# Optimization experiments

Measured on AMD Instinct MI355X. Metric: run time of the kernel, lower is better.

The kernel has to match this reference:

```python
import jax, jax.numpy as jnp
import numpy as np
from jax import lax

D = 768
H = 12
L = 12
FF = 4 * D
SCALE = D ** -0.5  # NOTE: original scales by embed_dim**-0.5, not head_dim**-0.5
LN_EPS = 1e-5


def _layernorm(x, g, b):
    mu = jnp.mean(x, axis=-1, keepdims=True)
    var = jnp.mean(jnp.square(x - mu), axis=-1, keepdims=True)
    return (x - mu) * lax.rsqrt(var + LN_EPS) * g + b


def setup_inputs() -> dict:
    key = jax.random.key(0)
    ks = jax.random.split(key, 8)
    x = jax.random.normal(ks[0], (4, 1024, D), dtype=jnp.float32)
    s = 0.02
    Wq = s * jax.random.normal(ks[1], (L, D, D), dtype=jnp.float32)
    Wv = s * jax.random.normal(ks[2], (L, D, D), dtype=jnp.float32)
    Wo = s * jax.random.normal(ks[3], (L, D, D), dtype=jnp.float32)
    W1 = s * jax.random.normal(ks[4], (L, D, FF), dtype=jnp.float32)
    W2 = s * jax.random.normal(ks[5], (L, FF, D), dtype=jnp.float32)
    zD = jnp.zeros((L, D), dtype=jnp.float32)
    return {
        'x': x,
        'ln1_g': jnp.ones((L, D), jnp.float32), 'ln1_b': zD,
        'Wq': Wq, 'bq': zD, 'Wv': Wv, 'bv': zD, 'Wo': Wo, 'bo': zD,
        'ln2_g': jnp.ones((L, D), jnp.float32), 'ln2_b': zD,
        'W1': W1, 'b1': jnp.zeros((L, FF), jnp.float32),
        'W2': W2, 'b2': zD,
    }


def _block(x, p):
    ln1_g, ln1_b, Wq, bq, Wv, bv, Wo, bo, ln2_g, ln2_b, W1, b1, W2, b2 = p
    B, T, _ = x.shape
    h = _layernorm(x, ln1_g, ln1_b)
    # Faithful to source: scores use query vs VALUE (fc_k output is dead code)
    q = (h @ Wq + bq).reshape(B, T, H, D // H)
    v = (h @ Wv + bv).reshape(B, T, H, D // H)
    scores = jnp.einsum('blhd,bthd->bhlt', q, v) * SCALE
    probs = jax.nn.softmax(scores, axis=-1)
    ctx = jnp.einsum('bhlt,bthd->blhd', probs, v).reshape(B, T, D)
    skip = x + ctx @ Wo + bo
    h2 = _layernorm(skip, ln2_g, ln2_b)
    ff = jax.nn.gelu(h2 @ W1 + b1, approximate=False) @ W2 + b2
    return skip + ff


def reference(x, ln1_g, ln1_b, Wq, bq, Wv, bv, Wo, bo, ln2_g, ln2_b, W1, b1, W2, b2):
    params = (ln1_g, ln1_b, Wq, bq, Wv, bv, Wo, bo, ln2_g, ln2_b, W1, b1, W2, b2)
    out, _ = lax.scan(lambda c, p: (_block(c, p), None), x, params)
    return out
```

## Files before the change

### kernel.cpp

```cpp
#include <hip/hip_runtime.h>
#include <math.h>

#define BB 4
#define TT 1024
#define DD 768
#define HH 12
#define DH 64
#define FF2 3072
#define NL 12
#define MM (BB * TT)
#define SCALE 0.03608439182435161f
#define LN_EPS 1e-5f

typedef __attribute__((ext_vector_type(8))) short bf16x8;
typedef __attribute__((ext_vector_type(4))) float f32x4;

__device__ __forceinline__ ushort f2b(float x) {
    uint u = __float_as_uint(x);
    uint r = (u + 0x7fffu + ((u >> 16) & 1u)) >> 16;
    return (ushort)r;
}
__device__ __forceinline__ float b2f(ushort h) { return __uint_as_float(((uint)h) << 16); }

__device__ __forceinline__ float gelu_exact(float x) {
    return 0.5f * x * (1.0f + erff(x * 0.70710678118654752440f));
}

__device__ __forceinline__ int swz(int r, int q) {
    return 4 * r + ((q ^ (r & 3) ^ ((r >> 2) & 3)) & 3);
}

__device__ __forceinline__ void gl_lds16(const ushort* g, ushort* l) {
    __builtin_amdgcn_global_load_lds(
        (__attribute__((address_space(1))) void*)(g),
        (__attribute__((address_space(3))) void*)(l), 16, 0, 0);
}

__global__ __launch_bounds__(256) void ln_kernel(const float* __restrict__ x,
                                                 const float* __restrict__ g,
                                                 const float* __restrict__ b,
                                                 ushort* __restrict__ out) {
    const int r = blockIdx.x;
    const int tid = threadIdx.x;
    const float* xr = x + (size_t)r * DD;
    float v0 = xr[tid], v1 = xr[tid + 256], v2 = xr[tid + 512];

    __shared__ float red[256];
    red[tid] = v0 + v1 + v2;
    __syncthreads();
    for (int off = 128; off > 0; off >>= 1) {
        if (tid < off) red[tid] += red[tid + off];
        __syncthreads();
    }
    float mu = red[0] * (1.0f / DD);
    __syncthreads();

    float d0 = v0 - mu, d1 = v1 - mu, d2 = v2 - mu;
    red[tid] = d0 * d0 + d1 * d1 + d2 * d2;
    __syncthreads();
    for (int off = 128; off > 0; off >>= 1) {
        if (tid < off) red[tid] += red[tid + off];
        __syncthreads();
    }
    float rstd = rsqrtf(red[0] * (1.0f / DD) + LN_EPS);

    ushort* outr = out + (size_t)r * DD;
    outr[tid]       = f2b(d0 * rstd * g[tid]       + b[tid]);
    outr[tid + 256] = f2b(d1 * rstd * g[tid + 256] + b[tid + 256]);
    outr[tid + 512] = f2b(d2 * rstd * g[tid + 512] + b[tid + 512]);
}

__global__ __launch_bounds__(256) void tconv(const float* __restrict__ W,
                                             ushort* __restrict__ Wt,
                                             int R, int C) {
    __shared__ float t[32][33];
    const int tx = threadIdx.x, ty = threadIdx.y;
    const int gr = blockIdx.y * 32, gc = blockIdx.x * 32;
#pragma unroll
    for (int i = 0; i < 4; ++i)
        t[ty + 8 * i][tx] = W[(size_t)(gr + ty + 8 * i) * C + gc + tx];
    __syncthreads();
#pragma unroll
    for (int i = 0; i < 4; ++i)
        Wt[(size_t)(gc + ty + 8 * i) * R + gr + tx] = f2b(t[tx][ty + 8 * i]);
}

__global__ __launch_bounds__(256) void vtrans(const ushort* __restrict__ V,
                                              ushort* __restrict__ Vt) {
    __shared__ ushort t[32][34];
    const int tx = threadIdx.x, ty = threadIdx.y;
    const int t0 = blockIdx.x * 32;
    const int d0 = blockIdx.y * 32;
    const int bh = blockIdx.z;
    const int b = bh / HH, h = bh % HH;
    const ushort* src = V + ((size_t)(b * TT + t0)) * DD + h * DH + d0;
#pragma unroll
    for (int i = 0; i < 4; ++i)
        t[ty + 8 * i][tx] = src[(size_t)(ty + 8 * i) * DD + tx];
    __syncthreads();
    ushort* dst = Vt + ((size_t)bh * DH + d0) * TT + t0;
#pragma unroll
    for (int i = 0; i < 4; ++i)
        dst[(size_t)(ty + 8 * i) * TT + tx] = t[tx][ty + 8 * i];
}

template <int BN, int EPI, bool OBF16>
__global__ __launch_bounds__(256) void mfma_gemm(const ushort* __restrict__ A,
                                                 const ushort* __restrict__ Wt,
                                                 const float* __restrict__ bias,
                                                 const float* __restrict__ res,
                                                 void* __restrict__ Cout,
                                                 int M, int N, int K) {
    constexpr int BM = 128;
    constexpr int ACH = BM * 4;
    constexpr int BCH = BN * 4;
    constexpr int CH  = ACH + BCH;
    constexpr int PT  = CH / 256;
    constexpr int NI = (BN == 128) ? 4 : 2;
    constexpr int NJ = 4;

    __shared__ __align__(16) ushort Tile[3][CH * 8];

    const int tid = threadIdx.x;
    const int lane = tid & 63, wave = tid >> 6;
    const int wm = (BN == 128) ? (wave & 1) * 64 : wave * 32;
    const int wn = (BN == 128) ? (wave >> 1) * 64 : 0;
    const int m0 = blockIdx.y * BM, n0 = blockIdx.x * BN;

    f32x4 acc[NI][NJ];
#pragma unroll
    for (int i = 0; i < NI; ++i)
#pragma unroll
        for (int j = 0; j < NJ; ++j) acc[i][j] = (f32x4){0.f, 0.f, 0.f, 0.f};

    const ushort* gsrc[PT];
#pragma unroll
    for (int s = 0; s < PT; ++s) {
        int c = tid + 256 * s;
        if (c < ACH) {
            int r = c >> 2, qs = c & 3;
            int ql = qs ^ (r & 3) ^ ((r >> 2) & 3);
            gsrc[s] = A + (size_t)(m0 + r) * K + ql * 8;
        } else {
            int cb = c - ACH;
            int r = cb >> 2, qs = cb & 3;
            int ql = qs ^ (r & 3) ^ ((r >> 2) & 3);
            gsrc[s] = Wt + (size_t)(n0 + r) * K + ql * 8;
        }
    }

    auto stage = [&](int bi, int k0) {
#pragma unroll
        for (int s = 0; s < PT; ++s)
            gl_lds16(gsrc[s] + k0, &Tile[bi][(tid + 256 * s) * 8]);
    };

    const int q = lane >> 4;
    int ca[NI], cb[NJ];
#pragma unroll
    for (int i = 0; i < NI; ++i) { int r = wm + i * 16 + (lane & 15); ca[i] = swz(r, q); }
#pragma unroll
    for (int j = 0; j < NJ; ++j) { int r = wn + j * 16 + (lane & 15); cb[j] = ACH + swz(r, q); }

    const int NT = K / 32;
    stage(0, 0);
    stage(1, 32);

    for (int t = 0; t < NT; ++t) {
        if (t < NT - 1) {
            if constexpr (PT == 3) asm volatile("s_waitcnt vmcnt(3) lgkmcnt(0)" ::: "memory");
            else                   asm volatile("s_waitcnt vmcnt(4) lgkmcnt(0)" ::: "memory");
        } else {
            asm volatile("s_waitcnt vmcnt(0) lgkmcnt(0)" ::: "memory");
        }
        __builtin_amdgcn_s_barrier();

        if (t + 2 < NT) stage((t + 2) % 3, (t + 2) * 32);

        const int bi = t % 3;
        bf16x8 af[NI], bfr[NJ];
#pragma unroll
        for (int i = 0; i < NI; ++i) af[i] = *(const bf16x8*)(&Tile[bi][ca[i] * 8]);
#pragma unroll
        for (int j = 0; j < NJ; ++j) bfr[j] = *(const bf16x8*)(&Tile[bi][cb[j] * 8]);
#pragma unroll
        for (int i = 0; i < NI; ++i)
#pragma unroll
            for (int j = 0; j < NJ; ++j)
                acc[i][j] = __builtin_amdgcn_mfma_f32_16x16x32_bf16(af[i], bfr[j], acc[i][j], 0, 0, 0);
    }

    const int col = lane & 15, rq = (lane >> 4) * 4;
#pragma unroll
    for (int j = 0; j < NJ; ++j) {
        const int n = n0 + wn + j * 16 + col;
        const float bj = bias[n];
#pragma unroll
        for (int i = 0; i < NI; ++i) {
#pragma unroll
            for (int r4 = 0; r4 < 4; ++r4) {
                const int m = m0 + wm + i * 16 + rq + r4;
                float v = acc[i][j][r4] + bj;
                if (EPI == 1) v += res[(size_t)m * N + n];
                if (EPI == 2) v = gelu_exact(v);
                if (OBF16) ((ushort*)Cout)[(size_t)m * N + n] = f2b(v);
                else       ((float*)Cout)[(size_t)m * N + n] = v;
            }
        }
    }
}

__global__ __launch_bounds__(256) void attn_mfma(const ushort* __restrict__ Q,
                                                 const ushort* __restrict__ V,
                                                 const ushort* __restrict__ Vt,
                                                 ushort* __restrict__ Ctx) {
    const int qt = blockIdx.x & 7;
    const int h  = (blockIdx.x >> 3) % HH;
    const int b  = blockIdx.x / (8 * HH);
    const int tid = threadIdx.x;
    const int lane = tid & 63, wave = tid >> 6;
    const int l15 = lane & 15, lq = lane >> 4;

    __shared__ __align__(16) ushort Vs [64][72];
    __shared__ __align__(16) ushort Vts[64][72];
    __shared__ __align__(16) ushort Ps [128][72];

    const int q0 = qt * 128;
    const int wq = wave * 32;

    bf16x8 qf[2][2];
    const ushort* Qb = Q + ((size_t)(b * TT + q0 + wq)) * DD + h * DH;
#pragma unroll
    for (int i = 0; i < 2; ++i)
#pragma unroll
        for (int ks = 0; ks < 2; ++ks)
            qf[i][ks] = *(const bf16x8*)(Qb + (size_t)(16 * i + l15) * DD + 32 * ks + lq * 8);

    const ushort* Vb  = V  + ((size_t)b * TT) * DD + h * DH;
    const ushort* Vtb = Vt + ((size_t)(b * HH + h) * DH) * TT;

    f32x4 O[2][4];
    float lsum[2][4];
#pragma unroll
    for (int i = 0; i < 2; ++i)
#pragma unroll
        for (int j = 0; j < 4; ++j) O[i][j] = (f32x4){0.f, 0.f, 0.f, 0.f};
#pragma unroll
    for (int i = 0; i < 2; ++i)
#pragma unroll
        for (int r = 0; r < 4; ++r) lsum[i][r] = 0.f;

    uint4 va[2], vta[2];
#pragma unroll
    for (int c = 0; c < 2; ++c) {
        int idx = tid + 256 * c;
        int row = idx >> 3, q8 = idx & 7;
        va[c]  = *(const uint4*)(Vb  + (size_t)row * DD + q8 * 8);
        vta[c] = *(const uint4*)(Vtb + (size_t)row * TT + q8 * 8);
    }

    for (int t = 0; t < 16; ++t) {
        __syncthreads();
#pragma unroll
        for (int c = 0; c < 2; ++c) {
            int idx = tid + 256 * c;
            int row = idx >> 3, q8 = idx & 7;
            *(uint4*)(&Vs[row][q8 * 8])  = va[c];
            *(uint4*)(&Vts[row][q8 * 8]) = vta[c];
        }
        __syncthreads();

        const int tn = ((t + 1) & 15) * 64;
#pragma unroll
        for (int c = 0; c < 2; ++c) {
            int idx = tid + 256 * c;
            int row = idx >> 3, q8 = idx & 7;
            va[c]  = *(const uint4*)(Vb  + (size_t)(tn + row) * DD + q8 * 8);
            vta[c] = *(const uint4*)(Vtb + (size_t)row * TT + tn + q8 * 8);
        }

        f32x4 s[2][4];
#pragma unroll
        for (int i = 0; i < 2; ++i)
#pragma unroll
            for (int j = 0; j < 4; ++j) s[i][j] = (f32x4){0.f, 0.f, 0.f, 0.f};
#pragma unroll
        for (int ks = 0; ks < 2; ++ks)
#pragma unroll
            for (int j = 0; j < 4; ++j) {
                bf16x8 vf = *(const bf16x8*)(&Vs[16 * j + l15][32 * ks + lq * 8]);
                s[0][j] = __builtin_amdgcn_mfma_f32_16x16x32_bf16(qf[0][ks], vf, s[0][j], 0, 0, 0);
                s[1][j] = __builtin_amdgcn_mfma_f32_16x16x32_bf16(qf[1][ks], vf, s[1][j], 0, 0, 0);
            }

#pragma unroll
        for (int i = 0; i < 2; ++i)
#pragma unroll
            for (int j = 0; j < 4; ++j)
#pragma unroll
                for (int r = 0; r < 4; ++r) {
                    float p = __expf(s[i][j][r] * SCALE);
                    ushort pb = f2b(p);
                    lsum[i][r] += b2f(pb);
                    Ps[wq + 16 * i + lq * 4 + r][16 * j + l15] = pb;
                }

#pragma unroll
        for (int ks = 0; ks < 2; ++ks) {
            bf16x8 pf0 = *(const bf16x8*)(&Ps[wq + l15][32 * ks + lq * 8]);
            bf16x8 pf1 = *(const bf16x8*)(&Ps[wq + 16 + l15][32 * ks + lq * 8]);
#pragma unroll
            for (int jd = 0; jd < 4; ++jd) {
                bf16x8 vtf = *(const bf16x8*)(&Vts[16 * jd + l15][32 * ks + lq * 8]);
                O[0][jd] = __builtin_amdgcn_mfma_f32_16x16x32_bf16(pf0, vtf, O[0][jd], 0, 0, 0);
                O[1][jd] = __builtin_amdgcn_mfma_f32_16x16x32_bf16(pf1, vtf, O[1][jd], 0, 0, 0);
            }
        }
    }

#pragma unroll
    for (int i = 0; i < 2; ++i)
#pragma unroll
        for (int r = 0; r < 4; ++r) {
            float l = lsum[i][r];
            l += __shfl_xor(l, 1);
            l += __shfl_xor(l, 2);
            l += __shfl_xor(l, 4);
            l += __shfl_xor(l, 8);
            lsum[i][r] = 1.0f / l;
        }

    ushort* Cb = Ctx + ((size_t)(b * TT + q0 + wq)) * DD + h * DH;
#pragma unroll
    for (int i = 0; i < 2; ++i)
#pragma unroll
        for (int r = 0; r < 4; ++r) {
            const int row = 16 * i + lq * 4 + r;
            const float inv = lsum[i][r];
#pragma unroll
            for (int jd = 0; jd < 4; ++jd)
                Cb[(size_t)row * DD + 16 * jd + l15] = f2b(O[i][jd][r] * inv);
        }
}

extern "C" void kernel_launch(void* const* d_in, const int* in_sizes, int n_in,
                              void* d_out, int out_size, void* d_ws, size_t ws_size,
                              hipStream_t stream) {
    const float* x_in  = (const float*)d_in[0];
    const float* ln1_g = (const float*)d_in[1];
    const float* ln1_b = (const float*)d_in[2];
    const float* Wq    = (const float*)d_in[3];
    const float* bq    = (const float*)d_in[4];
    const float* Wv    = (const float*)d_in[5];
    const float* bv    = (const float*)d_in[6];
    const float* Wo    = (const float*)d_in[7];
    const float* bo    = (const float*)d_in[8];
    const float* ln2_g = (const float*)d_in[9];
    const float* ln2_b = (const float*)d_in[10];
    const float* W1    = (const float*)d_in[11];
    const float* b1    = (const float*)d_in[12];
    const float* W2    = (const float*)d_in[13];
    const float* b2    = (const float*)d_in[14];

    float* x = (float*)d_out;
    ushort* h   = (ushort*)d_ws;
    ushort* qb  = h   + (size_t)MM * DD;
    ushort* vb  = qb  + (size_t)MM * DD;
    ushort* ctx = vb  + (size_t)MM * DD;
    ushort* h2  = ctx + (size_t)MM * DD;
    ushort* a1  = h2  + (size_t)MM * DD;
    ushort* Wtq = a1  + (size_t)MM * FF2;
    ushort* Wtv = Wtq + (size_t)DD * DD;
    ushort* Wto = Wtv + (size_t)DD * DD;
    ushort* Wt1 = Wto + (size_t)DD * DD;
    ushort* Wt2 = Wt1 + (size_t)DD * FF2;
    ushort* vt  = h;

    hipMemcpyAsync(x, x_in, (size_t)MM * DD * sizeof(float),
                   hipMemcpyDeviceToDevice, stream);

    const dim3 blk(256);
    const dim3 t32(32, 8);
    const dim3 gD(12, 32);
    const dim3 gF(24, 32);

    for (int l = 0; l < NL; ++l) {
        const float* Wq_l = Wq + (size_t)l * DD * DD;
        const float* Wv_l = Wv + (size_t)l * DD * DD;
        const float* Wo_l = Wo + (size_t)l * DD * DD;
        const float* W1_l = W1 + (size_t)l * DD * FF2;
        const float* W2_l = W2 + (size_t)l * FF2 * DD;

        tconv<<<dim3(24, 24), t32, 0, stream>>>(Wq_l, Wtq, DD, DD);
        tconv<<<dim3(24, 24), t32, 0, stream>>>(Wv_l, Wtv, DD, DD);
        tconv<<<dim3(24, 24), t32, 0, stream>>>(Wo_l, Wto, DD, DD);
        tconv<<<dim3(96, 24), t32, 0, stream>>>(W1_l, Wt1, DD, FF2);
        tconv<<<dim3(24, 96), t32, 0, stream>>>(W2_l, Wt2, FF2, DD);

        ln_kernel<<<MM, blk, 0, stream>>>(x, ln1_g + l * DD, ln1_b + l * DD, h);

        mfma_gemm<64, 0, true><<<gD, blk, 0, stream>>>(h, Wtq, bq + l * DD, nullptr, qb, MM, DD, DD);
        mfma_gemm<64, 0, true><<<gD, blk, 0, stream>>>(h, Wtv, bv + l * DD, nullptr, vb, MM, DD, DD);

        vtrans<<<dim3(TT / 32, DH / 32, BB * HH), t32, 0, stream>>>(vb, vt);

        attn_mfma<<<BB * HH * (TT / 128), blk, 0, stream>>>(qb, vb, vt, ctx);

        mfma_gemm<64, 1, false><<<gD, blk, 0, stream>>>(ctx, Wto, bo + l * DD, x, x, MM, DD, DD);

        ln_kernel<<<MM, blk, 0, stream>>>(x, ln2_g + l * DD, ln2_b + l * DD, h2);

        mfma_gemm<128, 2, true><<<gF, blk, 0, stream>>>(h2, Wt1, b1 + l * FF2, nullptr, a1, MM, FF2, DD);

        mfma_gemm<64, 1, false><<<gD, blk, 0, stream>>>(a1, Wt2, b2 + l * DD, x, x, MM, DD, FF2);
    }
}
```

Before: 3.025 ms.

## Fuse Q/V projections, retile GEMMs with XCD-aware block mapping, halve attention tile

Merges the Q and V projection GEMMs into one launch over a concatenated N=1536 output, with a split epilogue writing to two buffers. GEMM tiles become 64x64 for the D-wide GEMMs, with a 1D grid remapped so neighbouring tiles land on the same XCD for L2 locality. Attention uses 64-query blocks (twice as many workgroups), double-buffered V tiles, and one fewer barrier per step. The aim is more parallelism and fewer launches, at the cost of less reuse per tile and more total tile loads.

After: 3.291 ms. 1.09x slower.

```diff
diff --git a/kernel.cpp b/kernel.cpp
--- a/kernel.cpp
+++ b/kernel.cpp
@@ -104,28 +104,38 @@
         dst[(size_t)(ty + 8 * i) * TT + tx] = t[tx][ty + 8 * i];
 }
 
-template <int BN, int EPI, bool OBF16>
+template <int BM, int BN, int GX, int GY, int EPI, bool OBF16>
 __global__ __launch_bounds__(256) void mfma_gemm(const ushort* __restrict__ A,
                                                  const ushort* __restrict__ Wt,
                                                  const float* __restrict__ bias,
+                                                 const float* __restrict__ bias2,
                                                  const float* __restrict__ res,
                                                  void* __restrict__ Cout,
+                                                 void* __restrict__ Cout2,
                                                  int M, int N, int K) {
-    constexpr int BM = 128;
     constexpr int ACH = BM * 4;
     constexpr int BCH = BN * 4;
     constexpr int CH  = ACH + BCH;
     constexpr int PT  = CH / 256;
-    constexpr int NI = (BN == 128) ? 4 : 2;
-    constexpr int NJ = 4;
+    constexpr int WM  = (BM == 128 && BN == 64) ? 4 : 2;
+    constexpr int WN  = 4 / WM;
+    constexpr int NI  = BM / (WM * 16);
+    constexpr int NJ  = BN / (WN * 16);
+    constexpr int HX  = GX / 2;
+    constexpr int HY  = GY / 4;
 
     __shared__ __align__(16) ushort Tile[3][CH * 8];
+
+    const int lin = blockIdx.x;
+    const int xcd = lin & 7, inner = lin >> 3;
+    const int bx = (xcd & 1) * HX + inner % HX;
+    const int by = (xcd >> 1) * HY + inner / HX;
 
     const int tid = threadIdx.x;
     const int lane = tid & 63, wave = tid >> 6;
-    const int wm = (BN == 128) ? (wave & 1) * 64 : wave * 32;
-    const int wn = (BN == 128) ? (wave >> 1) * 64 : 0;
-    const int m0 = blockIdx.y * BM, n0 = blockIdx.x * BN;
+    const int wm = (wave % WM) * (NI * 16);
+    const int wn = (wave / WM) * (NJ * 16);
+    const int m0 = by * BM, n0 = bx * BN;
 
     f32x4 acc[NI][NJ];
 #pragma unroll
@@ -168,8 +178,9 @@
 
     for (int t = 0; t < NT; ++t) {
         if (t < NT - 1) {
-            if constexpr (PT == 3) asm volatile("s_waitcnt vmcnt(3) lgkmcnt(0)" ::: "memory");
-            else                   asm volatile("s_waitcnt vmcnt(4) lgkmcnt(0)" ::: "memory");
+            if constexpr (PT == 2)      asm volatile("s_waitcnt vmcnt(2) lgkmcnt(0)" ::: "memory");
+            else if constexpr (PT == 3) asm volatile("s_waitcnt vmcnt(3) lgkmcnt(0)" ::: "memory");
+            else                        asm volatile("s_waitcnt vmcnt(4) lgkmcnt(0)" ::: "memory");
         } else {
             asm volatile("s_waitcnt vmcnt(0) lgkmcnt(0)" ::: "memory");
         }
@@ -194,7 +205,7 @@
 #pragma unroll
     for (int j = 0; j < NJ; ++j) {
         const int n = n0 + wn + j * 16 + col;
-        const float bj = bias[n];
+        const float bj = (EPI == 3) ? (n < DD ? bias[n] : bias2[n - DD]) : bias[n];
 #pragma unroll
         for (int i = 0; i < NI; ++i) {
 #pragma unroll
@@ -203,8 +214,15 @@
                 float v = acc[i][j][r4] + bj;
                 if (EPI == 1) v += res[(size_t)m * N + n];
                 if (EPI == 2) v = gelu_exact(v);
-                if (OBF16) ((ushort*)Cout)[(size_t)m * N + n] = f2b(v);
-                else       ((float*)Cout)[(size_t)m * N + n] = v;
+                if (EPI == 3) {
+                    ushort* o = (n < DD) ? ((ushort*)Cout  + (size_t)m * DD + n)
+                                         : ((ushort*)Cout2 + (size_t)m * DD + (n - DD));
+                    *o = f2b(v);
+                } else if (OBF16) {
+                    ((ushort*)Cout)[(size_t)m * N + n] = f2b(v);
+                } else {
+                    ((float*)Cout)[(size_t)m * N + n] = v;
+                }
             }
         }
     }
@@ -214,41 +232,36 @@
                                                  const ushort* __restrict__ V,
                                                  const ushort* __restrict__ Vt,
                                                  ushort* __restrict__ Ctx) {
-    const int qt = blockIdx.x & 7;
-    const int h  = (blockIdx.x >> 3) % HH;
-    const int b  = blockIdx.x / (8 * HH);
+    const int x = blockIdx.x;
+    const int bh = ((x >> 7) << 3) | (x & 7);
+    const int qt = (x >> 3) & 15;
+    const int b = bh / HH, h = bh % HH;
     const int tid = threadIdx.x;
     const int lane = tid & 63, wave = tid >> 6;
     const int l15 = lane & 15, lq = lane >> 4;
 
-    __shared__ __align__(16) ushort Vs [64][72];
-    __shared__ __align__(16) ushort Vts[64][72];
-    __shared__ __align__(16) ushort Ps [128][72];
-
-    const int q0 = qt * 128;
-    const int wq = wave * 32;
-
-    bf16x8 qf[2][2];
+    __shared__ __align__(16) ushort Vs [2][64][72];
+    __shared__ __align__(16) ushort Vts[2][64][72];
+    __shared__ __align__(16) ushort Ps [64][72];
+
+    const int q0 = qt * 64;
+    const int wq = wave * 16;
+
+    bf16x8 qf[2];
     const ushort* Qb = Q + ((size_t)(b * TT + q0 + wq)) * DD + h * DH;
 #pragma unroll
-    for (int i = 0; i < 2; ++i)
-#pragma unroll
-        for (int ks = 0; ks < 2; ++ks)
-            qf[i][ks] = *(const bf16x8*)(Qb + (size_t)(16 * i + l15) * DD + 32 * ks + lq * 8);
+    for (int ks = 0; ks < 2; ++ks)
+        qf[ks] = *(const bf16x8*)(Qb + (size_t)l15 * DD + 32 * ks + lq * 8);
 
     const ushort* Vb  = V  + ((size_t)b * TT) * DD + h * DH;
     const ushort* Vtb = Vt + ((size_t)(b * HH + h) * DH) * TT;
 
-    f32x4 O[2][4];
-    float lsum[2][4];
-#pragma unroll
-    for (int i = 0; i < 2; ++i)
-#pragma unroll
-        for (int j = 0; j < 4; ++j) O[i][j] = (f32x4){0.f, 0.f, 0.f, 0.f};
-#pragma unroll
-    for (int i = 0; i < 2; ++i)
-#pragma unroll
-        for (int r = 0; r < 4; ++r) lsum[i][r] = 0.f;
+    f32x4 O[4];
+    float lsum[4];
+#pragma unroll
+    for (int j = 0; j < 4; ++j) O[j] = (f32x4){0.f, 0.f, 0.f, 0.f};
+#pragma unroll
+    for (int r = 0; r < 4; ++r) lsum[r] = 0.f;
 
     uint4 va[2], vta[2];
 #pragma unroll
@@ -260,87 +273,78 @@
     }
 
     for (int t = 0; t < 16; ++t) {
-        __syncthreads();
+        const int bi = t & 1;
 #pragma unroll
         for (int c = 0; c < 2; ++c) {
             int idx = tid + 256 * c;
             int row = idx >> 3, q8 = idx & 7;
-            *(uint4*)(&Vs[row][q8 * 8])  = va[c];
-            *(uint4*)(&Vts[row][q8 * 8]) = vta[c];
+            *(uint4*)(&Vs[bi][row][q8 * 8])  = va[c];
+            *(uint4*)(&Vts[bi][row][q8 * 8]) = vta[c];
         }
         __syncthreads();
 
-        const int tn = ((t + 1) & 15) * 64;
-#pragma unroll
-        for (int c = 0; c < 2; ++c) {
-            int idx = tid + 256 * c;
-            int row = idx >> 3, q8 = idx & 7;
-            va[c]  = *(const uint4*)(Vb  + (size_t)(tn + row) * DD + q8 * 8);
-            vta[c] = *(const uint4*)(Vtb + (size_t)row * TT + tn + q8 * 8);
-        }
-
-        f32x4 s[2][4];
-#pragma unroll
-        for (int i = 0; i < 2; ++i)
-#pragma unroll
-            for (int j = 0; j < 4; ++j) s[i][j] = (f32x4){0.f, 0.f, 0.f, 0.f};
+        if (t < 15) {
+            const int tn = (t + 1) * 64;
+#pragma unroll
+            for (int c = 0; c < 2; ++c) {
+                int idx = tid + 256 * c;
+                int row = idx >> 3, q8 = idx & 7;
+                va[c]  = *(const uint4*)(Vb  + (size_t)(tn + row) * DD + q8 * 8);
+                vta[c] = *(const uint4*)(Vtb + (size_t)row * TT + tn + q8 * 8);
+            }
+        }
+
+        f32x4 s[4];
+#pragma unroll
+        for (int j = 0; j < 4; ++j) s[j] = (f32x4){0.f, 0.f, 0.f, 0.f};
 #pragma unroll
         for (int ks = 0; ks < 2; ++ks)
 #pragma unroll
             for (int j = 0; j < 4; ++j) {
-                bf16x8 vf = *(const bf16x8*)(&Vs[16 * j + l15][32 * ks + lq * 8]);
-                s[0][j] = __builtin_amdgcn_mfma_f32_16x16x32_bf16(qf[0][ks], vf, s[0][j], 0, 0, 0);
-                s[1][j] = __builtin_amdgcn_mfma_f32_16x16x32_bf16(qf[1][ks], vf, s[1][j], 0, 0, 0);
+                bf16x8 vf = *(const bf16x8*)(&Vs[bi][16 * j + l15][32 * ks + lq * 8]);
+                s[j] = __builtin_amdgcn_mfma_f32_16x16x32_bf16(qf[ks], vf, s[j], 0, 0, 0);
             }
 
 #pragma unroll
-        for (int i = 0; i < 2; ++i)
-#pragma unroll
-            for (int j = 0; j < 4; ++j)
-#pragma unroll
-                for (int r = 0; r < 4; ++r) {
-                    float p = __expf(s[i][j][r] * SCALE);
-                    ushort pb = f2b(p);
-                    lsum[i][r] += b2f(pb);
-                    Ps[wq + 16 * i + lq * 4 + r][16 * j + l15] = pb;
-                }
+        for (int j = 0; j < 4; ++j)
+#pragma unroll
+            for (int r = 0; r < 4; ++r) {
+                float p = __expf(s[j][r] * SCALE);
+                ushort pb = f2b(p);
+                lsum[r] += b2f(pb);
+                Ps[wq + lq * 4 + r][16 * j + l15] = pb;
+            }
 
 #pragma unroll
         for (int ks = 0; ks < 2; ++ks) {
-            bf16x8 pf0 = *(const bf16x8*)(&Ps[wq + l15][32 * ks + lq * 8]);
-            bf16x8 pf1 = *(const bf16x8*)(&Ps[wq + 16 + l15][32 * ks + lq * 8]);
+            bf16x8 pf = *(const bf16x8*)(&Ps[wq + l15][32 * ks + lq * 8]);
 #pragma unroll
             for (int jd = 0; jd < 4; ++jd) {
-                bf16x8 vtf = *(const bf16x8*)(&Vts[16 * jd + l15][32 * ks + lq * 8]);
-                O[0][jd] = __builtin_amdgcn_mfma_f32_16x16x32_bf16(pf0, vtf, O[0][jd], 0, 0, 0);
-                O[1][jd] = __builtin_amdgcn_mfma_f32_16x16x32_bf16(pf1, vtf, O[1][jd], 0, 0, 0);
+                bf16x8 vtf = *(const bf16x8*)(&Vts[bi][16 * jd + l15][32 * ks + lq * 8]);
+                O[jd] = __builtin_amdgcn_mfma_f32_16x16x32_bf16(pf, vtf, O[jd], 0, 0, 0);
             }
         }
     }
 
 #pragma unroll
-    for (int i = 0; i < 2; ++i)
-#pragma unroll
-        for (int r = 0; r < 4; ++r) {
-            float l = lsum[i][r];
-            l += __shfl_xor(l, 1);
-            l += __shfl_xor(l, 2);
-            l += __shfl_xor(l, 4);
-            l += __shfl_xor(l, 8);
-            lsum[i][r] = 1.0f / l;
-        }
+    for (int r = 0; r < 4; ++r) {
+        float l = lsum[r];
+        l += __shfl_xor(l, 1);
+        l += __shfl_xor(l, 2);
+        l += __shfl_xor(l, 4);
+        l += __shfl_xor(l, 8);
+        lsum[r] = 1.0f / l;
+    }
 
     ushort* Cb = Ctx + ((size_t)(b * TT + q0 + wq)) * DD + h * DH;
 #pragma unroll
-    for (int i = 0; i < 2; ++i)
-#pragma unroll
-        for (int r = 0; r < 4; ++r) {
-            const int row = 16 * i + lq * 4 + r;
-            const float inv = lsum[i][r];
-#pragma unroll
-            for (int jd = 0; jd < 4; ++jd)
-                Cb[(size_t)row * DD + 16 * jd + l15] = f2b(O[i][jd][r] * inv);
-        }
+    for (int r = 0; r < 4; ++r) {
+        const int row = lq * 4 + r;
+        const float inv = lsum[r];
+#pragma unroll
+        for (int jd = 0; jd < 4; ++jd)
+            Cb[(size_t)row * DD + 16 * jd + l15] = f2b(O[jd][r] * inv);
+    }
 }
 
 extern "C" void kernel_launch(void* const* d_in, const int* in_sizes, int n_in,
@@ -381,8 +385,6 @@
 
     const dim3 blk(256);
     const dim3 t32(32, 8);
-    const dim3 gD(12, 32);
-    const dim3 gF(24, 32);
 
     for (int l = 0; l < NL; ++l) {
         const float* Wq_l = Wq + (size_t)l * DD * DD;
@@ -399,19 +401,22 @@
 
         ln_kernel<<<MM, blk, 0, stream>>>(x, ln1_g + l * DD, ln1_b + l * DD, h);
 
-        mfma_gemm<64, 0, true><<<gD, blk, 0, stream>>>(h, Wtq, bq + l * DD, nullptr, qb, MM, DD, DD);
-        mfma_gemm<64, 0, true><<<gD, blk, 0, stream>>>(h, Wtv, bv + l * DD, nullptr, vb, MM, DD, DD);
+        mfma_gemm<64, 64, 24, 64, 3, true><<<dim3(1536), blk, 0, stream>>>(
+            h, Wtq, bq + l * DD, bv + l * DD, nullptr, qb, vb, MM, 2 * DD, DD);
 
         vtrans<<<dim3(TT / 32, DH / 32, BB * HH), t32, 0, stream>>>(vb, vt);
 
-        attn_mfma<<<BB * HH * (TT / 128), blk, 0, stream>>>(qb, vb, vt, ctx);
-
-        mfma_gemm<64, 1, false><<<gD, blk, 0, stream>>>(ctx, Wto, bo + l * DD, x, x, MM, DD, DD);
+        attn_mfma<<<dim3(BB * HH * (TT / 64)), blk, 0, stream>>>(qb, vb, vt, ctx);
+
+        mfma_gemm<64, 64, 12, 64, 1, false><<<dim3(768), blk, 0, stream>>>(
+            ctx, Wto, bo + l * DD, nullptr, x, x, nullptr, MM, DD, DD);
 
         ln_kernel<<<MM, blk, 0, stream>>>(x, ln2_g + l * DD, ln2_b + l * DD, h2);
 
-        mfma_gemm<128, 2, true><<<gF, blk, 0, stream>>>(h2, Wt1, b1 + l * FF2, nullptr, a1, MM, FF2, DD);
-
-        mfma_gemm<64, 1, false><<<gD, blk, 0, stream>>>(a1, Wt2, b2 + l * DD, x, x, MM, DD, FF2);
-    }
-}
+        mfma_gemm<128, 128, 24, 32, 2, true><<<dim3(768), blk, 0, stream>>>(
+            h2, Wt1, b1 + l * FF2, nullptr, nullptr, a1, nullptr, MM, FF2, DD);
+
+        mfma_gemm<64, 64, 12, 64, 1, false><<<dim3(768), blk, 0, stream>>>(
+            a1, Wt2, b2 + l * DD, nullptr, x, x, nullptr, MM, DD, FF2);
+    }
+}
```
